# Kernel optimization log

Measured on AMD Instinct MI355X. Metric: run time of the kernel, lower is better.

Reference implementation:

```python
import jax, jax.numpy as jnp
import numpy as np

N_NODES = 100000
IN_CH = 256
OUT_CH = 128
HID = 2 * OUT_CH  # 256
N_EDGES = 1600000


def gcn_conv(x, src, dst, W, b, num_nodes):
    """PyG GCNConv: add self-loops, symmetric deg^-1/2 normalization,
    linear transform, scatter-add aggregation, plus bias."""
    h = x @ W  # [N, F_out]
    loop = jnp.arange(num_nodes, dtype=src.dtype)
    src_f = jnp.concatenate([src, loop])
    dst_f = jnp.concatenate([dst, loop])
    ones = jnp.ones(src_f.shape[0], dtype=h.dtype)
    deg = jax.ops.segment_sum(ones, dst_f, num_segments=num_nodes)
    dis = jnp.where(deg > 0, jax.lax.rsqrt(deg), 0.0)
    norm = dis[src_f] * dis[dst_f]  # [E+N]
    msg = h[src_f] * norm[:, None]  # [E+N, F_out]
    out = jax.ops.segment_sum(msg, dst_f, num_segments=num_nodes)
    return out + b


def setup_inputs() -> dict:
    key = jax.random.key(0)
    ks = jax.random.split(key, 8)
    x = jax.random.normal(ks[0], (N_NODES, IN_CH), dtype=jnp.float32)
    edge_index = jax.random.randint(ks[1], (2, N_EDGES), 0, N_NODES, dtype=jnp.int64 if jax.config.jax_enable_x64 else jnp.int32)
    s1 = 1.0 / np.sqrt(IN_CH)
    s2 = 1.0 / np.sqrt(HID)
    W1 = jax.random.uniform(ks[2], (IN_CH, HID), jnp.float32, -s1, s1)
    b1 = jnp.zeros((HID,), jnp.float32)
    W_mu = jax.random.uniform(ks[3], (HID, OUT_CH), jnp.float32, -s2, s2)
    b_mu = jnp.zeros((OUT_CH,), jnp.float32)
    W_lv = jax.random.uniform(ks[4], (HID, OUT_CH), jnp.float32, -s2, s2)
    b_lv = jnp.zeros((OUT_CH,), jnp.float32)
    return {"x": x, "edge_index": edge_index, "W1": W1, "b1": b1,
            "W_mu": W_mu, "b_mu": b_mu, "W_lv": W_lv, "b_lv": b_lv}


def reference(x, edge_index, W1, b1, W_mu, b_mu, W_lv, b_lv):
    src, dst = edge_index[0], edge_index[1]
    h = jax.nn.relu(gcn_conv(x, src, dst, W1, b1, N_NODES))
    mu = gcn_conv(h, src, dst, W_mu, b_mu, N_NODES)
    logvar = gcn_conv(h, src, dst, W_lv, b_lv, N_NODES)
    return (mu, logvar)
```

## Files before the change

kernel.cpp:

```cpp
#include <hip/hip_runtime.h>
#include <hip/hip_fp16.h>

#define N_NODES 100000
#define E_EDGES 1600000
#define F 256
#define LV_OFF 12800000
#define NBUK 782
#define EPB 8192
#define NBLK_BIN 196

typedef _Float16 half8 __attribute__((ext_vector_type(8)));
typedef _Float16 f16x4 __attribute__((ext_vector_type(4)));
typedef float    f32x4 __attribute__((ext_vector_type(4)));
typedef unsigned u32x4 __attribute__((ext_vector_type(4)));

__device__ __forceinline__ void fmix2(float& lo, float& hi, unsigned v) {
    asm("v_fma_mix_f32 %0, %2, 1.0, %0 op_sel_hi:[1,0,0]\n\t"
        "v_fma_mix_f32 %1, %2, 1.0, %1 op_sel:[1,0,0] op_sel_hi:[1,0,0]"
        : "+v"(lo), "+v"(hi) : "v"(v));
}

__device__ __forceinline__ void acc_row(float* a, half8 v) {
    u32x4 u = __builtin_bit_cast(u32x4, v);
    fmix2(a[0], a[1], u[0]);
    fmix2(a[2], a[3], u[1]);
    fmix2(a[4], a[5], u[2]);
    fmix2(a[6], a[7], u[3]);
}

__global__ void k_zero2(int* __restrict__ cnt, int* __restrict__ gcnt) {
    int i = blockIdx.x * 256 + threadIdx.x;
    if (i < N_NODES) cnt[i] = 0;
    if (i < NBUK) gcnt[i] = 0;
}

__global__ __launch_bounds__(256) void k_prep(
    const float* __restrict__ W1, const float* __restrict__ Wmu, const float* __restrict__ Wlv,
    _Float16* __restrict__ Wt1, _Float16* __restrict__ Wtc,
    const int* __restrict__ dst, int* __restrict__ gcnt, int* __restrict__ cbase,
    int* __restrict__ cnt)
{
    __shared__ int h[NBUK];
    int bid = blockIdx.x, tid = threadIdx.x;
    if (bid < 256) {
        int idx = bid * 256 + tid;
        int n = idx >> 8, k = idx & 255;
        Wt1[n * 256 + k] = (_Float16)W1[k * 256 + n];
        float wc = (n < 128) ? Wmu[k * 128 + n] : Wlv[k * 128 + (n - 128)];
        Wtc[n * 256 + k] = (_Float16)wc;
        return;
    }
    int blk = bid - 256;
    for (int b = tid; b < NBUK; b += 256) h[b] = 0;
    __syncthreads();
    int e0 = blk * EPB, e1 = min(e0 + EPB, E_EDGES);
    for (int e = e0 + tid; e < e1; e += 256) {
        int d = dst[e];
        atomicAdd(&h[d >> 7], 1);
        atomicAdd(&cnt[d], 1);
    }
    __syncthreads();
    for (int b = tid; b < NBUK; b += 256) {
        int c = h[b];
        cbase[blk * NBUK + b] = c ? atomicAdd(&gcnt[b], c) : 0;
    }
}

__global__ __launch_bounds__(1024) void k_scan_dis(const int* __restrict__ gcnt,
                                                   int* __restrict__ gbase,
                                                   const int* __restrict__ cnt,
                                                   float* __restrict__ dis) {
    int tid = threadIdx.x;
    if (blockIdx.x != 0) {
        int i = (blockIdx.x - 1) * 1024 + tid;
        if (i < N_NODES) dis[i] = rsqrtf((float)cnt[i] + 1.0f);
        return;
    }
    __shared__ int sd[1024];
    int v = (tid < NBUK) ? gcnt[tid] : 0;
    sd[tid] = v;
    __syncthreads();
    for (int off = 1; off < 1024; off <<= 1) {
        int t = (tid >= off) ? sd[tid - off] : 0;
        __syncthreads();
        sd[tid] += t;
        __syncthreads();
    }
    if (tid < NBUK) gbase[tid] = sd[tid] - v;
    if (tid == NBUK - 1) gbase[NBUK] = sd[tid];
}

__global__ __launch_bounds__(256) void k_binD(const unsigned long long* __restrict__ ebuf,
                                              const int* __restrict__ gbase,
                                              int* __restrict__ csr_src, int* __restrict__ row_off) {
    __shared__ int dh[128], dsc[128], dcur[128];
    int b = blockIdx.x, tid = threadIdx.x;
    if (tid < 128) dh[tid] = 0;
    __syncthreads();
    int s0 = gbase[b], s1 = gbase[b + 1];
    for (int i = s0 + tid; i < s1; i += 256)
        atomicAdd(&dh[(int)(ebuf[i] >> 32) & 127], 1);
    __syncthreads();
    if (tid < 128) dsc[tid] = dh[tid];
    __syncthreads();
    for (int off = 1; off < 128; off <<= 1) {
        int t = 0;
        if (tid < 128 && tid >= off) t = dsc[tid - off];
        __syncthreads();
        if (tid < 128) dsc[tid] += t;
        __syncthreads();
    }
    if (tid < 128) {
        int ex = dsc[tid] - dh[tid];
        dcur[tid] = ex;
        int node = b * 128 + tid;
        if (node < N_NODES) row_off[node] = s0 + ex;
    }
    if (b == 0 && tid == 128) row_off[N_NODES] = E_EDGES;
    __syncthreads();
    for (int i = s0 + tid; i < s1; i += 256) {
        unsigned long long ed = ebuf[i];
        int dl = (int)(ed >> 32) & 127;
        int lr = atomicAdd(&dcur[dl], 1);
        csr_src[s0 + lr] = (int)(ed & 0xFFFFFFFFull);
    }
}

template <typename TA>
__device__ __forceinline__ void gemm_tile(
    const TA* __restrict__ A, const _Float16* __restrict__ Bt,
    const float* __restrict__ dis, _Float16* __restrict__ G, int M,
    int m0, int tid, _Float16* Ah, _Float16* Bh)
{
    const int wave = tid >> 6, lane = tid & 63;
    const int wm   = wave & 1, wn = wave >> 1;
    const int lrow = lane & 15, kgrp = lane >> 4;

    f32x4 acc[4][4];
#pragma unroll
    for (int i = 0; i < 4; i++)
#pragma unroll
        for (int j = 0; j < 4; j++) acc[i][j] = (f32x4){0.f, 0.f, 0.f, 0.f};

    for (int kt = 0; kt < 256; kt += 64) {
        if constexpr (sizeof(TA) == 4) {
#pragma unroll
            for (int p = 0; p < 4; ++p) {
                int u = p * 512 + tid;
                int row = u >> 4, kq = u & 15;
                int gm = m0 + row; if (gm >= M) gm = M - 1;
                f32x4 v = __builtin_nontemporal_load(
                    reinterpret_cast<const f32x4*>((const float*)A + (size_t)gm * F + kt + kq * 4));
                f16x4 h4;
                h4[0] = (_Float16)v[0]; h4[1] = (_Float16)v[1];
                h4[2] = (_Float16)v[2]; h4[3] = (_Float16)v[3];
                *reinterpret_cast<f16x4*>(&Ah[row * 64 + ((kq * 4) ^ ((row & 7) << 3))]) = h4;
            }
        } else {
#pragma unroll
            for (int p = 0; p < 2; ++p) {
                int u = p * 512 + tid;
                int row = u >> 3, slot = u & 7;
                int gm = m0 + row; if (gm >= M) gm = M - 1;
                half8 v = __builtin_nontemporal_load(
                    reinterpret_cast<const half8*>((const _Float16*)A + (size_t)gm * F + kt + slot * 8));
                *reinterpret_cast<half8*>(&Ah[row * 64 + ((slot * 8) ^ ((row & 7) << 3))]) = v;
            }
        }
#pragma unroll
        for (int p = 0; p < 4; ++p) {
            int u = p * 512 + tid;
            int n = u >> 3, slot = u & 7;
            half8 v = *reinterpret_cast<const half8*>(Bt + (size_t)n * F + kt + slot * 8);
            *reinterpret_cast<half8*>(&Bh[n * 64 + ((slot * 8) ^ ((n & 7) << 3))]) = v;
        }
        __syncthreads();
#pragma unroll
        for (int ks = 0; ks < 2; ++ks) {
            int kk = ks * 32 + kgrp * 8;
            half8 ah[4];
#pragma unroll
            for (int i = 0; i < 4; ++i) {
                int row = wm * 64 + i * 16 + lrow;
                ah[i] = *reinterpret_cast<const half8*>(&Ah[row * 64 + (kk ^ ((row & 7) << 3))]);
            }
#pragma unroll
            for (int j = 0; j < 4; ++j) {
                int col = wn * 64 + j * 16 + lrow;
                half8 bh = *reinterpret_cast<const half8*>(&Bh[col * 64 + (kk ^ ((col & 7) << 3))]);
#pragma unroll
                for (int i = 0; i < 4; ++i)
                    acc[i][j] = __builtin_amdgcn_mfma_f32_16x16x32_f16(ah[i], bh, acc[i][j], 0, 0, 0);
            }
        }
        __syncthreads();
    }

#pragma unroll
    for (int i = 0; i < 4; ++i) {
#pragma unroll
        for (int r = 0; r < 4; ++r) {
            int m = m0 + wm * 64 + i * 16 + kgrp * 4 + r;
            if (m >= M) continue;
            float dv = dis[m];
#pragma unroll
            for (int j = 0; j < 4; ++j) {
                int n = wn * 64 + j * 16 + lrow;
                G[(size_t)m * F + n] = (_Float16)(acc[i][j][r] * dv);
            }
        }
    }
}

__global__ __launch_bounds__(512, 4) void k_gemm_binC(
    const float* __restrict__ A, const _Float16* __restrict__ Bt,
    const float* __restrict__ dis, _Float16* __restrict__ G, int M,
    const int* __restrict__ src, const int* __restrict__ dst,
    const int* __restrict__ gbase, const int* __restrict__ cbase,
    unsigned long long* __restrict__ ebuf)
{
    __shared__ _Float16 smem[128 * 64 + 256 * 64];
    int bid = blockIdx.x, tid = threadIdx.x;
    int r5 = bid % 5;
    if (r5 < 4) {
        int gid = (bid / 5) * 4 + r5;
        if (gid < 782)
            gemm_tile<float>(A, Bt, dis, G, M, gid * 128, tid, smem, smem + 128 * 64);
        return;
    }
    int* h2 = (int*)smem;
    int* bs = h2 + NBUK;
    int blk = bid / 5;
    for (int b = tid; b < NBUK; b += 512) {
        h2[b] = 0;
        bs[b] = gbase[b] + cbase[blk * NBUK + b];
    }
    __syncthreads();
    int e0 = blk * EPB, e1 = min(e0 + EPB, E_EDGES);
    for (int e = e0 + tid; e < e1; e += 512) {
        int d = dst[e];
        int b = d >> 7;
        int lr = atomicAdd(&h2[b], 1);
        ebuf[bs[b] + lr] = ((unsigned long long)(unsigned)d << 32) | (unsigned)src[e];
    }
}

__global__ __launch_bounds__(512, 4) void k_gemm_f16(
    const _Float16* __restrict__ A, const _Float16* __restrict__ Bt,
    const float* __restrict__ dis, _Float16* __restrict__ G, int M)
{
    __shared__ _Float16 smem[128 * 64 + 256 * 64];
    gemm_tile<_Float16>(A, Bt, dis, G, M, blockIdx.x * 128, threadIdx.x, smem, smem + 128 * 64);
}

template <int RELU>
__device__ __forceinline__ void aggregate_body(
    const _Float16* __restrict__ g, const int* __restrict__ row_off,
    const int* __restrict__ csr_src, const float* __restrict__ dis,
    const float* __restrict__ bmu, const float* __restrict__ blv,
    _Float16* __restrict__ hout, float* __restrict__ out)
{
    int d = blockIdx.x * 4 + (threadIdx.x >> 6);
    int lane = threadIdx.x & 63;
    int hf = lane >> 5, lp = lane & 31;
    const half8* g8 = reinterpret_cast<const half8*>(g);
    float a0[8] = {0,0,0,0,0,0,0,0}, a1[8] = {0,0,0,0,0,0,0,0};
    if (hf == 0) {
        half8 sv = g8[(size_t)d * 32 + lp];
#pragma unroll
        for (int k = 0; k < 8; k++) a0[k] = (float)sv[k];
    }
    int j0 = row_off[d], j1 = row_off[d + 1];
    int j = j0 + hf;
    for (; j + 10 < j1; j += 12) {
        int s0 = csr_src[j],     s1 = csr_src[j + 2], s2 = csr_src[j + 4];
        int s3 = csr_src[j + 6], s4 = csr_src[j + 8], s5 = csr_src[j + 10];
        half8 v0 = g8[(size_t)s0 * 32 + lp];
        half8 v1 = g8[(size_t)s1 * 32 + lp];
        half8 v2 = g8[(size_t)s2 * 32 + lp];
        half8 v3 = g8[(size_t)s3 * 32 + lp];
        half8 v4 = g8[(size_t)s4 * 32 + lp];
        half8 v5 = g8[(size_t)s5 * 32 + lp];
        acc_row(a0, v0); acc_row(a1, v1);
        acc_row(a0, v2); acc_row(a1, v3);
        acc_row(a0, v4); acc_row(a1, v5);
    }
    for (; j + 2 < j1; j += 4) {
        int sA = csr_src[j], sB = csr_src[j + 2];
        half8 vA = g8[(size_t)sA * 32 + lp];
        half8 vB = g8[(size_t)sB * 32 + lp];
        acc_row(a0, vA); acc_row(a1, vB);
    }
    if (j < j1) {
        int sA = csr_src[j];
        half8 vA = g8[(size_t)sA * 32 + lp];
        acc_row(a0, vA);
    }
#pragma unroll
    for (int k = 0; k < 8; k++) {
        a0[k] += a1[k];
        a0[k] += __shfl_xor(a0[k], 32);
    }
    float dd = dis[d];
    if (RELU) {
        int c = lp * 8 + hf * 4;
        float4 bb = *reinterpret_cast<const float4*>(bmu + c);
        f16x4 o;
        o[0] = (_Float16)fmaxf(fmaf(dd, a0[hf * 4 + 0], bb.x), 0.0f);
        o[1] = (_Float16)fmaxf(fmaf(dd, a0[hf * 4 + 1], bb.y), 0.0f);
        o[2] = (_Float16)fmaxf(fmaf(dd, a0[hf * 4 + 2], bb.z), 0.0f);
        o[3] = (_Float16)fmaxf(fmaf(dd, a0[hf * 4 + 3], bb.w), 0.0f);
        *reinterpret_cast<f16x4*>(hout + (size_t)d * F + c) = o;
    } else {
        int ch = lp * 8 + hf * 4;
        float va = a0[hf * 4 + 0], vb = a0[hf * 4 + 1], vc = a0[hf * 4 + 2], vd = a0[hf * 4 + 3];
        if (ch < 128) {
            float4 bb = *reinterpret_cast<const float4*>(bmu + ch);
            f32x4 o = {fmaf(dd, va, bb.x), fmaf(dd, vb, bb.y),
                       fmaf(dd, vc, bb.z), fmaf(dd, vd, bb.w)};
            __builtin_nontemporal_store(o, reinterpret_cast<f32x4*>(out + (size_t)d * 128 + ch));
        } else {
            int c2 = ch - 128;
            float4 bb = *reinterpret_cast<const float4*>(blv + c2);
            f32x4 o = {fmaf(dd, va, bb.x), fmaf(dd, vb, bb.y),
                       fmaf(dd, vc, bb.z), fmaf(dd, vd, bb.w)};
            __builtin_nontemporal_store(o, reinterpret_cast<f32x4*>(out + LV_OFF + (size_t)d * 128 + c2));
        }
    }
}

__global__ __launch_bounds__(256) void k_aggregate_relu(
    const _Float16* __restrict__ g, const int* __restrict__ row_off,
    const int* __restrict__ csr_src, const float* __restrict__ dis,
    const float* __restrict__ b, _Float16* __restrict__ h)
{
    aggregate_body<1>(g, row_off, csr_src, dis, b, nullptr, h, nullptr);
}

__global__ __launch_bounds__(256) void k_aggregate_out(
    const _Float16* __restrict__ g, const int* __restrict__ row_off,
    const int* __restrict__ csr_src, const float* __restrict__ dis,
    const float* __restrict__ bmu, const float* __restrict__ blv,
    float* __restrict__ out)
{
    aggregate_body<0>(g, row_off, csr_src, dis, bmu, blv, nullptr, out);
}

extern "C" void kernel_launch(void* const* d_in, const int* in_sizes, int n_in,
                              void* d_out, int out_size, void* d_ws, size_t ws_size,
                              hipStream_t stream) {
    const float* x   = (const float*)d_in[0];
    const int*   ei  = (const int*)d_in[1];
    const int*   src = ei;
    const int*   dst = ei + E_EDGES;
    const float* W1  = (const float*)d_in[2];
    const float* b1  = (const float*)d_in[3];
    const float* Wmu = (const float*)d_in[4];
    const float* bmu = (const float*)d_in[5];
    const float* Wlv = (const float*)d_in[6];
    const float* blv = (const float*)d_in[7];
    float* out = (float*)d_out;

    char* ws = (char*)d_ws;
    size_t o = 0;
    auto carve = [&](size_t bytes) -> char* {
        char* p = ws + o;
        o = (o + bytes + 1023) & ~(size_t)1023;
        return p;
    };
    float*    dis     = (float*)   carve(400000);
    int*      cnt     = (int*)     carve(400000);
    int*      row_off = (int*)     carve(400004);
    int*      gcnt    = (int*)     carve(NBUK * 4);
    int*      gbase   = (int*)     carve((NBUK + 1) * 4);
    int*      cbase   = (int*)     carve((size_t)NBLK_BIN * NBUK * 4);
    _Float16* Wt1     = (_Float16*)carve(131072);
    _Float16* Wtc     = (_Float16*)carve(131072);
    int*      csr_src = (int*)     carve((size_t)E_EDGES * 4);
    unsigned long long* ebuf = (unsigned long long*)carve((size_t)E_EDGES * 8);
    _Float16* g       = (_Float16*)carve((size_t)N_NODES * F * 2);
    (void)ws_size;

    _Float16* h16 = (_Float16*)(out + LV_OFF);

    k_zero2   <<<(N_NODES + 255) / 256, 256, 0, stream>>>(cnt, gcnt);
    k_prep    <<<256 + NBLK_BIN, 256, 0, stream>>>(W1, Wmu, Wlv, Wt1, Wtc, dst, gcnt, cbase, cnt);
    k_scan_dis<<<99, 1024, 0, stream>>>(gcnt, gbase, cnt, dis);
    k_gemm_binC<<<980, 512, 0, stream>>>(x, Wt1, dis, g, N_NODES, src, dst, gbase, cbase, ebuf);
    k_binD     <<<NBUK, 256, 0, stream>>>(ebuf, gbase, csr_src, row_off);

    k_aggregate_relu<<<N_NODES / 4, 256, 0, stream>>>(g, row_off, csr_src, dis, b1, h16);

    k_gemm_f16<<<782, 512, 0, stream>>>(h16, Wtc, dis, g, N_NODES);
    k_aggregate_out<<<N_NODES / 4, 256, 0, stream>>>(g, row_off, csr_src, dis, bmu, blv, out);
}
```

Baseline: 421.2 us.

## Fuse first-layer aggregation with second GEMM via LDS-resident hidden tile

Each block of the new fused kernel gathers and aggregates 128 rows of layer-1 features, applies bias, ReLU and normalization, and stores the fp16 result in a 64KB LDS tile. It then multiplies that tile by the concatenated mu/logvar weights with MFMA. This removes the global round-trip of the hidden activation and one kernel launch. The large LDS footprint and serial 16-rows-per-wave gather reduce occupancy and memory-latency hiding for the gather-bound aggregation phase, and an extra workspace buffer is used.

```diff
diff --git a/kernel.cpp b/kernel.cpp
--- a/kernel.cpp
+++ b/kernel.cpp
@@ -126,9 +126,8 @@
     }
 }
 
-template <typename TA>
-__device__ __forceinline__ void gemm_tile(
-    const TA* __restrict__ A, const _Float16* __restrict__ Bt,
+__device__ __forceinline__ void gemm_tile_f32(
+    const float* __restrict__ A, const _Float16* __restrict__ Bt,
     const float* __restrict__ dis, _Float16* __restrict__ G, int M,
     int m0, int tid, _Float16* Ah, _Float16* Bh)
 {
@@ -143,29 +142,17 @@
         for (int j = 0; j < 4; j++) acc[i][j] = (f32x4){0.f, 0.f, 0.f, 0.f};
 
     for (int kt = 0; kt < 256; kt += 64) {
-        if constexpr (sizeof(TA) == 4) {
-#pragma unroll
-            for (int p = 0; p < 4; ++p) {
-                int u = p * 512 + tid;
-                int row = u >> 4, kq = u & 15;
-                int gm = m0 + row; if (gm >= M) gm = M - 1;
-                f32x4 v = __builtin_nontemporal_load(
-                    reinterpret_cast<const f32x4*>((const float*)A + (size_t)gm * F + kt + kq * 4));
-                f16x4 h4;
-                h4[0] = (_Float16)v[0]; h4[1] = (_Float16)v[1];
-                h4[2] = (_Float16)v[2]; h4[3] = (_Float16)v[3];
-                *reinterpret_cast<f16x4*>(&Ah[row * 64 + ((kq * 4) ^ ((row & 7) << 3))]) = h4;
-            }
-        } else {
-#pragma unroll
-            for (int p = 0; p < 2; ++p) {
-                int u = p * 512 + tid;
-                int row = u >> 3, slot = u & 7;
-                int gm = m0 + row; if (gm >= M) gm = M - 1;
-                half8 v = __builtin_nontemporal_load(
-                    reinterpret_cast<const half8*>((const _Float16*)A + (size_t)gm * F + kt + slot * 8));
-                *reinterpret_cast<half8*>(&Ah[row * 64 + ((slot * 8) ^ ((row & 7) << 3))]) = v;
-            }
+#pragma unroll
+        for (int p = 0; p < 4; ++p) {
+            int u = p * 512 + tid;
+            int row = u >> 4, kq = u & 15;
+            int gm = m0 + row; if (gm >= M) gm = M - 1;
+            f32x4 v = __builtin_nontemporal_load(
+                reinterpret_cast<const f32x4*>(A + (size_t)gm * F + kt + kq * 4));
+            f16x4 h4;
+            h4[0] = (_Float16)v[0]; h4[1] = (_Float16)v[1];
+            h4[2] = (_Float16)v[2]; h4[3] = (_Float16)v[3];
+            *reinterpret_cast<f16x4*>(&Ah[row * 64 + ((kq * 4) ^ ((row & 7) << 3))]) = h4;
         }
 #pragma unroll
         for (int p = 0; p < 4; ++p) {
@@ -225,7 +212,7 @@
     if (r5 < 4) {
         int gid = (bid / 5) * 4 + r5;
         if (gid < 782)
-            gemm_tile<float>(A, Bt, dis, G, M, gid * 128, tid, smem, smem + 128 * 64);
+            gemm_tile_f32(A, Bt, dis, G, M, gid * 128, tid, smem, smem + 128 * 64);
         return;
     }
     int* h2 = (int*)smem;
@@ -245,20 +232,132 @@
     }
 }
 
-__global__ __launch_bounds__(512, 4) void k_gemm_f16(
-    const _Float16* __restrict__ A, const _Float16* __restrict__ Bt,
-    const float* __restrict__ dis, _Float16* __restrict__ G, int M)
+__global__ __launch_bounds__(512, 4) void k_agg_gemm(
+    const _Float16* __restrict__ g1, const int* __restrict__ row_off,
+    const int* __restrict__ csr_src, const float* __restrict__ dis,
+    const float* __restrict__ b1, const _Float16* __restrict__ Bt,
+    _Float16* __restrict__ G2, int M)
 {
-    __shared__ _Float16 smem[128 * 64 + 256 * 64];
-    gemm_tile<_Float16>(A, Bt, dis, G, M, blockIdx.x * 128, threadIdx.x, smem, smem + 128 * 64);
-}
-
-template <int RELU>
-__device__ __forceinline__ void aggregate_body(
+    __shared__ _Float16 HT[128 * 256];
+    __shared__ _Float16 Bs[256 * 32];
+    const int tid  = threadIdx.x;
+    const int m0   = blockIdx.x * 128;
+    const int wave = tid >> 6, lane = tid & 63;
+    const int hf   = lane >> 5, lp = lane & 31;
+    const half8* g8 = reinterpret_cast<const half8*>(g1);
+
+    for (int it = 0; it < 16; ++it) {
+        int r  = wave * 16 + it;
+        int gr = m0 + r;
+        float a0[8] = {0,0,0,0,0,0,0,0}, a1[8] = {0,0,0,0,0,0,0,0};
+        if (gr < M) {
+            if (hf == 0) {
+                half8 sv = g8[(size_t)gr * 32 + lp];
+#pragma unroll
+                for (int k = 0; k < 8; k++) a0[k] = (float)sv[k];
+            }
+            int j0 = row_off[gr], j1 = row_off[gr + 1];
+            int j = j0 + hf;
+            for (; j + 10 < j1; j += 12) {
+                int s0 = csr_src[j],     s1 = csr_src[j + 2], s2 = csr_src[j + 4];
+                int s3 = csr_src[j + 6], s4 = csr_src[j + 8], s5 = csr_src[j + 10];
+                half8 v0 = g8[(size_t)s0 * 32 + lp];
+                half8 v1 = g8[(size_t)s1 * 32 + lp];
+                half8 v2 = g8[(size_t)s2 * 32 + lp];
+                half8 v3 = g8[(size_t)s3 * 32 + lp];
+                half8 v4 = g8[(size_t)s4 * 32 + lp];
+                half8 v5 = g8[(size_t)s5 * 32 + lp];
+                acc_row(a0, v0); acc_row(a1, v1);
+                acc_row(a0, v2); acc_row(a1, v3);
+                acc_row(a0, v4); acc_row(a1, v5);
+            }
+            for (; j + 2 < j1; j += 4) {
+                int sA = csr_src[j], sB = csr_src[j + 2];
+                half8 vA = g8[(size_t)sA * 32 + lp];
+                half8 vB = g8[(size_t)sB * 32 + lp];
+                acc_row(a0, vA); acc_row(a1, vB);
+            }
+            if (j < j1) {
+                int sA = csr_src[j];
+                half8 vA = g8[(size_t)sA * 32 + lp];
+                acc_row(a0, vA);
+            }
+        }
+#pragma unroll
+        for (int k = 0; k < 8; k++) {
+            a0[k] += a1[k];
+            a0[k] += __shfl_xor(a0[k], 32);
+        }
+        int c = lp * 8 + hf * 4;
+        f16x4 o = (f16x4){(_Float16)0, (_Float16)0, (_Float16)0, (_Float16)0};
+        if (gr < M) {
+            float dd = dis[gr];
+            float4 bb = *reinterpret_cast<const float4*>(b1 + c);
+            o[0] = (_Float16)fmaxf(fmaf(dd, a0[hf * 4 + 0], bb.x), 0.0f);
+            o[1] = (_Float16)fmaxf(fmaf(dd, a0[hf * 4 + 1], bb.y), 0.0f);
+            o[2] = (_Float16)fmaxf(fmaf(dd, a0[hf * 4 + 2], bb.z), 0.0f);
+            o[3] = (_Float16)fmaxf(fmaf(dd, a0[hf * 4 + 3], bb.w), 0.0f);
+        }
+        *reinterpret_cast<f16x4*>(&HT[r * 256 + (c ^ ((r & 7) << 3))]) = o;
+    }
+    __syncthreads();
+
+    const int wm = wave & 1, wn = wave >> 1;
+    const int lrow = lane & 15, kgrp = lane >> 4;
+    f32x4 acc[4][4];
+#pragma unroll
+    for (int i = 0; i < 4; i++)
+#pragma unroll
+        for (int j = 0; j < 4; j++) acc[i][j] = (f32x4){0.f, 0.f, 0.f, 0.f};
+
+    for (int kt = 0; kt < 256; kt += 32) {
+#pragma unroll
+        for (int p = 0; p < 2; ++p) {
+            int u = p * 512 + tid;
+            int n = u >> 2, slot = u & 3;
+            half8 v = *reinterpret_cast<const half8*>(Bt + (size_t)n * F + kt + slot * 8);
+            *reinterpret_cast<half8*>(&Bs[n * 32 + ((slot * 8) ^ ((n & 3) << 3))]) = v;
+        }
+        __syncthreads();
+        int kk = kgrp * 8;
+        half8 ah[4];
+#pragma unroll
+        for (int i = 0; i < 4; ++i) {
+            int row = wm * 64 + i * 16 + lrow;
+            ah[i] = *reinterpret_cast<const half8*>(&HT[row * 256 + ((kt + kk) ^ ((row & 7) << 3))]);
+        }
+#pragma unroll
+        for (int j = 0; j < 4; ++j) {
+            int col = wn * 64 + j * 16 + lrow;
+            half8 bh = *reinterpret_cast<const half8*>(&Bs[col * 32 + (kk ^ ((col & 3) << 3))]);
+#pragma unroll
+            for (int i = 0; i < 4; ++i)
+                acc[i][j] = __builtin_amdgcn_mfma_f32_16x16x32_f16(ah[i], bh, acc[i][j], 0, 0, 0);
+        }
+        __syncthreads();
+    }
+
+#pragma unroll
+    for (int i = 0; i < 4; ++i) {
+#pragma unroll
+        for (int r = 0; r < 4; ++r) {
+            int m = m0 + wm * 64 + i * 16 + kgrp * 4 + r;
+            if (m >= M) continue;
+            float dv = dis[m];
+#pragma unroll
+            for (int j = 0; j < 4; ++j) {
+                int n = wn * 64 + j * 16 + lrow;
+                G2[(size_t)m * F + n] = (_Float16)(acc[i][j][r] * dv);
+            }
+        }
+    }
+}
+
+__global__ __launch_bounds__(256) void k_aggregate_out(
     const _Float16* __restrict__ g, const int* __restrict__ row_off,
     const int* __restrict__ csr_src, const float* __restrict__ dis,
     const float* __restrict__ bmu, const float* __restrict__ blv,
-    _Float16* __restrict__ hout, float* __restrict__ out)
+    float* __restrict__ out)
 {
     int d = blockIdx.x * 4 + (threadIdx.x >> 6);
     int lane = threadIdx.x & 63;
@@ -302,48 +401,20 @@
         a0[k] += __shfl_xor(a0[k], 32);
     }
     float dd = dis[d];
-    if (RELU) {
-        int c = lp * 8 + hf * 4;
-        float4 bb = *reinterpret_cast<const float4*>(bmu + c);
-        f16x4 o;
-        o[0] = (_Float16)fmaxf(fmaf(dd, a0[hf * 4 + 0], bb.x), 0.0f);
-        o[1] = (_Float16)fmaxf(fmaf(dd, a0[hf * 4 + 1], bb.y), 0.0f);
-        o[2] = (_Float16)fmaxf(fmaf(dd, a0[hf * 4 + 2], bb.z), 0.0f);
-        o[3] = (_Float16)fmaxf(fmaf(dd, a0[hf * 4 + 3], bb.w), 0.0f);
-        *reinterpret_cast<f16x4*>(hout + (size_t)d * F + c) = o;
+    int ch = lp * 8 + hf * 4;
+    float va = a0[hf * 4 + 0], vb = a0[hf * 4 + 1], vc = a0[hf * 4 + 2], vd = a0[hf * 4 + 3];
+    if (ch < 128) {
+        float4 bb = *reinterpret_cast<const float4*>(bmu + ch);
+        f32x4 o = {fmaf(dd, va, bb.x), fmaf(dd, vb, bb.y),
+                   fmaf(dd, vc, bb.z), fmaf(dd, vd, bb.w)};
+        __builtin_nontemporal_store(o, reinterpret_cast<f32x4*>(out + (size_t)d * 128 + ch));
     } else {
-        int ch = lp * 8 + hf * 4;
-        float va = a0[hf * 4 + 0], vb = a0[hf * 4 + 1], vc = a0[hf * 4 + 2], vd = a0[hf * 4 + 3];
-        if (ch < 128) {
-            float4 bb = *reinterpret_cast<const float4*>(bmu + ch);
-            f32x4 o = {fmaf(dd, va, bb.x), fmaf(dd, vb, bb.y),
-                       fmaf(dd, vc, bb.z), fmaf(dd, vd, bb.w)};
-            __builtin_nontemporal_store(o, reinterpret_cast<f32x4*>(out + (size_t)d * 128 + ch));
-        } else {
-            int c2 = ch - 128;
-            float4 bb = *reinterpret_cast<const float4*>(blv + c2);
-            f32x4 o = {fmaf(dd, va, bb.x), fmaf(dd, vb, bb.y),
-                       fmaf(dd, vc, bb.z), fmaf(dd, vd, bb.w)};
-            __builtin_nontemporal_store(o, reinterpret_cast<f32x4*>(out + LV_OFF + (size_t)d * 128 + c2));
-        }
-    }
-}
-
-__global__ __launch_bounds__(256) void k_aggregate_relu(
-    const _Float16* __restrict__ g, const int* __restrict__ row_off,
-    const int* __restrict__ csr_src, const float* __restrict__ dis,
-    const float* __restrict__ b, _Float16* __restrict__ h)
-{
-    aggregate_body<1>(g, row_off, csr_src, dis, b, nullptr, h, nullptr);
-}
-
-__global__ __launch_bounds__(256) void k_aggregate_out(
-    const _Float16* __restrict__ g, const int* __restrict__ row_off,
-    const int* __restrict__ csr_src, const float* __restrict__ dis,
-    const float* __restrict__ bmu, const float* __restrict__ blv,
-    float* __restrict__ out)
-{
-    aggregate_body<0>(g, row_off, csr_src, dis, bmu, blv, nullptr, out);
+        int c2 = ch - 128;
+        float4 bb = *reinterpret_cast<const float4*>(blv + c2);
+        f32x4 o = {fmaf(dd, va, bb.x), fmaf(dd, vb, bb.y),
+                   fmaf(dd, vc, bb.z), fmaf(dd, vd, bb.w)};
+        __builtin_nontemporal_store(o, reinterpret_cast<f32x4*>(out + LV_OFF + (size_t)d * 128 + c2));
+    }
 }
 
 extern "C" void kernel_launch(void* const* d_in, const int* in_sizes, int n_in,
@@ -378,19 +449,17 @@
     _Float16* Wtc     = (_Float16*)carve(131072);
     int*      csr_src = (int*)     carve((size_t)E_EDGES * 4);
     unsigned long long* ebuf = (unsigned long long*)carve((size_t)E_EDGES * 8);
-    _Float16* g       = (_Float16*)carve((size_t)N_NODES * F * 2);
+    _Float16* g1      = (_Float16*)carve((size_t)N_NODES * F * 2);
+    _Float16* g2      = (_Float16*)carve((size_t)N_NODES * F * 2);
     (void)ws_size;
-
-    _Float16* h16 = (_Float16*)(out + LV_OFF);
 
     k_zero2   <<<(N_NODES + 255) / 256, 256, 0, stream>>>(cnt, gcnt);
     k_prep    <<<256 + NBLK_BIN, 256, 0, stream>>>(W1, Wmu, Wlv, Wt1, Wtc, dst, gcnt, cbase, cnt);
     k_scan_dis<<<99, 1024, 0, stream>>>(gcnt, gbase, cnt, dis);
-    k_gemm_binC<<<980, 512, 0, stream>>>(x, Wt1, dis, g, N_NODES, src, dst, gbase, cbase, ebuf);
+    k_gemm_binC<<<980, 512, 0, stream>>>(x, Wt1, dis, g1, N_NODES, src, dst, gbase, cbase, ebuf);
     k_binD     <<<NBUK, 256, 0, stream>>>(ebuf, gbase, csr_src, row_off);
 
-    k_aggregate_relu<<<N_NODES / 4, 256, 0, stream>>>(g, row_off, csr_src, dis, b1, h16);
-
-    k_gemm_f16<<<782, 512, 0, stream>>>(h16, Wtc, dis, g, N_NODES);
-    k_aggregate_out<<<N_NODES / 4, 256, 0, stream>>>(g, row_off, csr_src, dis, bmu, blv, out);
-}
+    k_agg_gemm<<<782, 512, 0, stream>>>(g1, row_off, csr_src, dis, b1, Wtc, g2, N_NODES);
+
+    k_aggregate_out<<<N_NODES / 4, 256, 0, stream>>>(g2, row_off, csr_src, dis, bmu, blv, out);
+}
```

Result: slower. 431.9 us (+2.5%).

## Fuse CSR bucket build with first-layer aggregation; replace zero kernel with memsets

Applied to the files above, without the earlier changes.

The per-bucket CSR construction kernel and the first-layer ReLU aggregation are merged into one 1024-thread kernel. Each block builds the CSR for its 128 destination nodes and then aggregates those nodes right away, reading row offsets from shared memory and the freshly written csr_src while it is likely still in cache. This removes a kernel launch and one pass over row_off, but only 782 blocks do the aggregation, which may cut parallelism and latency hiding for the gather. The zeroing kernel is also replaced by two hipMemsetAsync calls.

```diff
diff --git a/kernel.cpp b/kernel.cpp
--- a/kernel.cpp
+++ b/kernel.cpp
@@ -26,12 +26,6 @@
     fmix2(a[2], a[3], u[1]);
     fmix2(a[4], a[5], u[2]);
     fmix2(a[6], a[7], u[3]);
-}
-
-__global__ void k_zero2(int* __restrict__ cnt, int* __restrict__ gcnt) {
-    int i = blockIdx.x * 256 + threadIdx.x;
-    if (i < N_NODES) cnt[i] = 0;
-    if (i < NBUK) gcnt[i] = 0;
 }
 
 __global__ __launch_bounds__(256) void k_prep(
@@ -88,42 +82,6 @@
     }
     if (tid < NBUK) gbase[tid] = sd[tid] - v;
     if (tid == NBUK - 1) gbase[NBUK] = sd[tid];
-}
-
-__global__ __launch_bounds__(256) void k_binD(const unsigned long long* __restrict__ ebuf,
-                                              const int* __restrict__ gbase,
-                                              int* __restrict__ csr_src, int* __restrict__ row_off) {
-    __shared__ int dh[128], dsc[128], dcur[128];
-    int b = blockIdx.x, tid = threadIdx.x;
-    if (tid < 128) dh[tid] = 0;
-    __syncthreads();
-    int s0 = gbase[b], s1 = gbase[b + 1];
-    for (int i = s0 + tid; i < s1; i += 256)
-        atomicAdd(&dh[(int)(ebuf[i] >> 32) & 127], 1);
-    __syncthreads();
-    if (tid < 128) dsc[tid] = dh[tid];
-    __syncthreads();
-    for (int off = 1; off < 128; off <<= 1) {
-        int t = 0;
-        if (tid < 128 && tid >= off) t = dsc[tid - off];
-        __syncthreads();
-        if (tid < 128) dsc[tid] += t;
-        __syncthreads();
-    }
-    if (tid < 128) {
-        int ex = dsc[tid] - dh[tid];
-        dcur[tid] = ex;
-        int node = b * 128 + tid;
-        if (node < N_NODES) row_off[node] = s0 + ex;
-    }
-    if (b == 0 && tid == 128) row_off[N_NODES] = E_EDGES;
-    __syncthreads();
-    for (int i = s0 + tid; i < s1; i += 256) {
-        unsigned long long ed = ebuf[i];
-        int dl = (int)(ed >> 32) & 127;
-        int lr = atomicAdd(&dcur[dl], 1);
-        csr_src[s0 + lr] = (int)(ed & 0xFFFFFFFFull);
-    }
 }
 
 template <typename TA>
@@ -253,12 +211,107 @@
     gemm_tile<_Float16>(A, Bt, dis, G, M, blockIdx.x * 128, threadIdx.x, smem, smem + 128 * 64);
 }
 
-template <int RELU>
-__device__ __forceinline__ void aggregate_body(
+__global__ __launch_bounds__(1024, 8) void k_binDagg(
+    const unsigned long long* __restrict__ ebuf, const int* __restrict__ gbase,
+    int* __restrict__ csr_src, int* __restrict__ row_off,
+    const _Float16* __restrict__ g1, const float* __restrict__ dis,
+    const float* __restrict__ b1, _Float16* __restrict__ hout)
+{
+    __shared__ int dh[128], dsc[128], dcur[128];
+    const int b = blockIdx.x, tid = threadIdx.x;
+    const int s0 = gbase[b], s1 = gbase[b + 1];
+
+    if (tid < 128) dh[tid] = 0;
+    __syncthreads();
+    for (int i = s0 + tid; i < s1; i += 1024)
+        atomicAdd(&dh[(int)(ebuf[i] >> 32) & 127], 1);
+    __syncthreads();
+    if (tid < 128) dsc[tid] = dh[tid];
+    __syncthreads();
+    for (int off = 1; off < 128; off <<= 1) {
+        int t = 0;
+        if (tid < 128 && tid >= off) t = dsc[tid - off];
+        __syncthreads();
+        if (tid < 128) dsc[tid] += t;
+        __syncthreads();
+    }
+    if (tid < 128) {
+        int ex = dsc[tid] - dh[tid];
+        dcur[tid] = ex;
+        int node = b * 128 + tid;
+        if (node < N_NODES) row_off[node] = s0 + ex;
+    }
+    if (b == 0 && tid == 128) row_off[N_NODES] = E_EDGES;
+    __syncthreads();
+    for (int i = s0 + tid; i < s1; i += 1024) {
+        unsigned long long ed = ebuf[i];
+        int dl = (int)(ed >> 32) & 127;
+        int lr = atomicAdd(&dcur[dl], 1);
+        csr_src[s0 + lr] = (int)(ed & 0xFFFFFFFFull);
+    }
+    __syncthreads();
+
+    const int wave = tid >> 6, lane = tid & 63;
+    const int hf = lane >> 5, lp = lane & 31;
+    const half8* g8 = reinterpret_cast<const half8*>(g1);
+    for (int it = 0; it < 8; ++it) {
+        int r  = wave * 8 + it;
+        int gr = b * 128 + r;
+        if (gr >= N_NODES) break;
+        float a0[8] = {0,0,0,0,0,0,0,0}, a1[8] = {0,0,0,0,0,0,0,0};
+        if (hf == 0) {
+            half8 sv = g8[(size_t)gr * 32 + lp];
+#pragma unroll
+            for (int k = 0; k < 8; k++) a0[k] = (float)sv[k];
+        }
+        int j0 = s0 + (dsc[r] - dh[r]), j1 = s0 + dsc[r];
+        int j = j0 + hf;
+        for (; j + 10 < j1; j += 12) {
+            int e0i = csr_src[j],     e1i = csr_src[j + 2], e2i = csr_src[j + 4];
+            int e3i = csr_src[j + 6], e4i = csr_src[j + 8], e5i = csr_src[j + 10];
+            half8 v0 = g8[(size_t)e0i * 32 + lp];
+            half8 v1 = g8[(size_t)e1i * 32 + lp];
+            half8 v2 = g8[(size_t)e2i * 32 + lp];
+            half8 v3 = g8[(size_t)e3i * 32 + lp];
+            half8 v4 = g8[(size_t)e4i * 32 + lp];
+            half8 v5 = g8[(size_t)e5i * 32 + lp];
+            acc_row(a0, v0); acc_row(a1, v1);
+            acc_row(a0, v2); acc_row(a1, v3);
+            acc_row(a0, v4); acc_row(a1, v5);
+        }
+        for (; j + 2 < j1; j += 4) {
+            int eA = csr_src[j], eB = csr_src[j + 2];
+            half8 vA = g8[(size_t)eA * 32 + lp];
+            half8 vB = g8[(size_t)eB * 32 + lp];
+            acc_row(a0, vA); acc_row(a1, vB);
+        }
+        if (j < j1) {
+            int eA = csr_src[j];
+            half8 vA = g8[(size_t)eA * 32 + lp];
+            acc_row(a0, vA);
+        }
+#pragma unroll
+        for (int k = 0; k < 8; k++) {
+            a0[k] += a1[k];
+            a0[k] += __shfl_xor(a0[k], 32);
+        }
+        float dd = dis[gr];
+        int c = lp * 8 + hf * 4;
+        float4 bb = *reinterpret_cast<const float4*>(b1 + c);
+        f16x4 o;
+        o[0] = (_Float16)fmaxf(fmaf(dd, a0[hf * 4 + 0], bb.x), 0.0f);
+        o[1] = (_Float16)fmaxf(fmaf(dd, a0[hf * 4 + 1], bb.y), 0.0f);
+        o[2] = (_Float16)fmaxf(fmaf(dd, a0[hf * 4 + 2], bb.z), 0.0f);
+        o[3] = (_Float16)fmaxf(fmaf(dd, a0[hf * 4 + 3], bb.w), 0.0f);
+        *reinterpret_cast<f16x4*>(hout + (size_t)gr * F + c) = o;
+    }
+}
+
+__global__ __launch_bounds__(256) void k_aggregate_out(
     const _Float16* __restrict__ g, const int* __restrict__ row_off,
     const int* __restrict__ csr_src, const float* __restrict__ dis,
     const float* __restrict__ bmu, const float* __restrict__ blv,
-    _Float16* __restrict__ hout, float* __restrict__ out)
+    float* __restrict__ out)
 {
     int d = blockIdx.x * 4 + (threadIdx.x >> 6);
     int lane = threadIdx.x & 63;
@@ -302,48 +355,20 @@
         a0[k] += __shfl_xor(a0[k], 32);
     }
     float dd = dis[d];
-    if (RELU) {
-        int c = lp * 8 + hf * 4;
-        float4 bb = *reinterpret_cast<const float4*>(bmu + c);
-        f16x4 o;
-        o[0] = (_Float16)fmaxf(fmaf(dd, a0[hf * 4 + 0], bb.x), 0.0f);
-        o[1] = (_Float16)fmaxf(fmaf(dd, a0[hf * 4 + 1], bb.y), 0.0f);
-        o[2] = (_Float16)fmaxf(fmaf(dd, a0[hf * 4 + 2], bb.z), 0.0f);
-        o[3] = (_Float16)fmaxf(fmaf(dd, a0[hf * 4 + 3], bb.w), 0.0f);
-        *reinterpret_cast<f16x4*>(hout + (size_t)d * F + c) = o;
+    int ch = lp * 8 + hf * 4;
+    float va = a0[hf * 4 + 0], vb = a0[hf * 4 + 1], vc = a0[hf * 4 + 2], vd = a0[hf * 4 + 3];
+    if (ch < 128) {
+        float4 bb = *reinterpret_cast<const float4*>(bmu + ch);
+        f32x4 o = {fmaf(dd, va, bb.x), fmaf(dd, vb, bb.y),
+                   fmaf(dd, vc, bb.z), fmaf(dd, vd, bb.w)};
+        __builtin_nontemporal_store(o, reinterpret_cast<f32x4*>(out + (size_t)d * 128 + ch));
     } else {
-        int ch = lp * 8 + hf * 4;
-        float va = a0[hf * 4 + 0], vb = a0[hf * 4 + 1], vc = a0[hf * 4 + 2], vd = a0[hf * 4 + 3];
-        if (ch < 128) {
-            float4 bb = *reinterpret_cast<const float4*>(bmu + ch);
-            f32x4 o = {fmaf(dd, va, bb.x), fmaf(dd, vb, bb.y),
-                       fmaf(dd, vc, bb.z), fmaf(dd, vd, bb.w)};
-            __builtin_nontemporal_store(o, reinterpret_cast<f32x4*>(out + (size_t)d * 128 + ch));
-        } else {
-            int c2 = ch - 128;
-            float4 bb = *reinterpret_cast<const float4*>(blv + c2);
-            f32x4 o = {fmaf(dd, va, bb.x), fmaf(dd, vb, bb.y),
-                       fmaf(dd, vc, bb.z), fmaf(dd, vd, bb.w)};
-            __builtin_nontemporal_store(o, reinterpret_cast<f32x4*>(out + LV_OFF + (size_t)d * 128 + c2));
-        }
-    }
-}
-
-__global__ __launch_bounds__(256) void k_aggregate_relu(
-    const _Float16* __restrict__ g, const int* __restrict__ row_off,
-    const int* __restrict__ csr_src, const float* __restrict__ dis,
-    const float* __restrict__ b, _Float16* __restrict__ h)
-{
-    aggregate_body<1>(g, row_off, csr_src, dis, b, nullptr, h, nullptr);
-}
-
-__global__ __launch_bounds__(256) void k_aggregate_out(
-    const _Float16* __restrict__ g, const int* __restrict__ row_off,
-    const int* __restrict__ csr_src, const float* __restrict__ dis,
-    const float* __restrict__ bmu, const float* __restrict__ blv,
-    float* __restrict__ out)
-{
-    aggregate_body<0>(g, row_off, csr_src, dis, bmu, blv, nullptr, out);
+        int c2 = ch - 128;
+        float4 bb = *reinterpret_cast<const float4*>(blv + c2);
+        f32x4 o = {fmaf(dd, va, bb.x), fmaf(dd, vb, bb.y),
+                   fmaf(dd, vc, bb.z), fmaf(dd, vd, bb.w)};
+        __builtin_nontemporal_store(o, reinterpret_cast<f32x4*>(out + LV_OFF + (size_t)d * 128 + c2));
+    }
 }
 
 extern "C" void kernel_launch(void* const* d_in, const int* in_sizes, int n_in,
@@ -383,14 +408,12 @@
 
     _Float16* h16 = (_Float16*)(out + LV_OFF);
 
-    k_zero2   <<<(N_NODES + 255) / 256, 256, 0, stream>>>(cnt, gcnt);
+    hipMemsetAsync(cnt, 0, 400000, stream);
+    hipMemsetAsync(gcnt, 0, NBUK * 4, stream);
     k_prep    <<<256 + NBLK_BIN, 256, 0, stream>>>(W1, Wmu, Wlv, Wt1, Wtc, dst, gcnt, cbase, cnt);
     k_scan_dis<<<99, 1024, 0, stream>>>(gcnt, gbase, cnt, dis);
     k_gemm_binC<<<980, 512, 0, stream>>>(x, Wt1, dis, g, N_NODES, src, dst, gbase, cbase, ebuf);
-    k_binD     <<<NBUK, 256, 0, stream>>>(ebuf, gbase, csr_src, row_off);
-
-    k_aggregate_relu<<<N_NODES / 4, 256, 0, stream>>>(g, row_off, csr_src, dis, b1, h16);
-
+    k_binDagg  <<<NBUK, 1024, 0, stream>>>(ebuf, gbase, csr_src, row_off, g, dis, b1, h16);
     k_gemm_f16<<<782, 512, 0, stream>>>(h16, Wtc, dis, g, N_NODES);
     k_aggregate_out<<<N_NODES / 4, 256, 0, stream>>>(g, row_off, csr_src, dis, bmu, blv, out);
 }
```

New measurement: 454.2 us. 1.08x slower.

## Load GEMM tiles directly into LDS with pre-swizzled global layouts

Applied to the files above, without the earlier changes.

Pre-swizzles the transposed weight matrices and the ReLU hidden output in global memory so each 64-wide K chunk already carries the LDS XOR bank swizzle. This lets the f16 GEMM paths use global_load_lds (direct global-to-LDS DMA) instead of loading through registers and then writing to shared memory. It also replaces the zeroing kernel with hipMemsetAsync calls. The change couples the producer layout to the consumer's LDS layout, and it relies on wave-contiguous 16-byte lane placement matching the swizzled rows.

```diff
diff --git a/kernel.cpp b/kernel.cpp
--- a/kernel.cpp
+++ b/kernel.cpp
@@ -28,10 +28,10 @@
     fmix2(a[6], a[7], u[3]);
 }
 
-__global__ void k_zero2(int* __restrict__ cnt, int* __restrict__ gcnt) {
-    int i = blockIdx.x * 256 + threadIdx.x;
-    if (i < N_NODES) cnt[i] = 0;
-    if (i < NBUK) gcnt[i] = 0;
+__device__ __forceinline__ void gload_lds16(const void* gsrc, void* ldst) {
+    __builtin_amdgcn_global_load_lds(
+        (const __attribute__((address_space(1))) void*)gsrc,
+        (__attribute__((address_space(3))) void*)ldst, 16, 0, 0);
 }
 
 __global__ __launch_bounds__(256) void k_prep(
@@ -45,9 +45,10 @@
     if (bid < 256) {
         int idx = bid * 256 + tid;
         int n = idx >> 8, k = idx & 255;
-        Wt1[n * 256 + k] = (_Float16)W1[k * 256 + n];
+        int ksw = (k & 192) | (((((k >> 3) & 7) ^ (n & 7))) << 3) | (k & 7);
+        Wt1[n * 256 + ksw] = (_Float16)W1[k * 256 + n];
         float wc = (n < 128) ? Wmu[k * 128 + n] : Wlv[k * 128 + (n - 128)];
-        Wtc[n * 256 + k] = (_Float16)wc;
+        Wtc[n * 256 + ksw] = (_Float16)wc;
         return;
     }
     int blk = bid - 256;
@@ -159,20 +160,21 @@
         } else {
 #pragma unroll
             for (int p = 0; p < 2; ++p) {
-                int u = p * 512 + tid;
+                int q = wave * 2 + p;
+                int u = q * 64 + lane;
                 int row = u >> 3, slot = u & 7;
                 int gm = m0 + row; if (gm >= M) gm = M - 1;
-                half8 v = __builtin_nontemporal_load(
-                    reinterpret_cast<const half8*>((const _Float16*)A + (size_t)gm * F + kt + slot * 8));
-                *reinterpret_cast<half8*>(&Ah[row * 64 + ((slot * 8) ^ ((row & 7) << 3))]) = v;
+                gload_lds16((const _Float16*)A + (size_t)gm * F + kt + slot * 8,
+                            Ah + (size_t)q * 512);
             }
         }
 #pragma unroll
         for (int p = 0; p < 4; ++p) {
-            int u = p * 512 + tid;
+            int q = wave * 4 + p;
+            int u = q * 64 + lane;
             int n = u >> 3, slot = u & 7;
-            half8 v = *reinterpret_cast<const half8*>(Bt + (size_t)n * F + kt + slot * 8);
-            *reinterpret_cast<half8*>(&Bh[n * 64 + ((slot * 8) ^ ((n & 7) << 3))]) = v;
+            gload_lds16(Bt + (size_t)n * F + kt + slot * 8,
+                        Bh + (size_t)q * 512);
         }
         __syncthreads();
 #pragma unroll
@@ -310,7 +312,8 @@
         o[1] = (_Float16)fmaxf(fmaf(dd, a0[hf * 4 + 1], bb.y), 0.0f);
         o[2] = (_Float16)fmaxf(fmaf(dd, a0[hf * 4 + 2], bb.z), 0.0f);
         o[3] = (_Float16)fmaxf(fmaf(dd, a0[hf * 4 + 3], bb.w), 0.0f);
-        *reinterpret_cast<f16x4*>(hout + (size_t)d * F + c) = o;
+        int csw = ((lp >> 3) << 6) | ((((lp & 7) ^ (d & 7))) << 3) | (hf * 4);
+        *reinterpret_cast<f16x4*>(hout + (size_t)d * F + csw) = o;
     } else {
         int ch = lp * 8 + hf * 4;
         float va = a0[hf * 4 + 0], vb = a0[hf * 4 + 1], vc = a0[hf * 4 + 2], vd = a0[hf * 4 + 3];
@@ -383,7 +386,8 @@
 
     _Float16* h16 = (_Float16*)(out + LV_OFF);
 
-    k_zero2   <<<(N_NODES + 255) / 256, 256, 0, stream>>>(cnt, gcnt);
+    hipMemsetAsync(cnt, 0, 400000, stream);
+    hipMemsetAsync(gcnt, 0, NBUK * 4, stream);
     k_prep    <<<256 + NBLK_BIN, 256, 0, stream>>>(W1, Wmu, Wlv, Wt1, Wtc, dst, gcnt, cbase, cnt);
     k_scan_dis<<<99, 1024, 0, stream>>>(gcnt, gbase, cnt, dis);
     k_gemm_binC<<<980, 512, 0, stream>>>(x, Wt1, dis, g, N_NODES, src, dst, gbase, cbase, ebuf);
```

Measured after the change: 419.9 us. About the same (-0.3%).
